# Kernel optimization log

Measured on AMD Instinct MI355X. Metric: run time of the kernel, lower is better.

Reference implementation:

```python
import jax, jax.numpy as jnp
import numpy as np

N_HEAD = 16

def setup_inputs() -> dict:
    key = jax.random.key(0)
    kx, kq, kk, kv, kp = jax.random.split(key, 5)
    B, T, C = 4, 2048, 1024
    scale = 1.0 / np.sqrt(C)
    x = jax.random.normal(kx, (B, T, C), dtype=jnp.float32)
    Wq = jax.random.normal(kq, (C, C), dtype=jnp.float32) * scale
    Wk = jax.random.normal(kk, (C, C), dtype=jnp.float32) * scale
    Wv = jax.random.normal(kv, (C, C), dtype=jnp.float32) * scale
    Wp = jax.random.normal(kp, (C, C), dtype=jnp.float32) * scale
    return {"x": x, "Wq": Wq, "Wk": Wk, "Wv": Wv, "Wp": Wp}

def reference(x, Wq, Wk, Wv, Wp):
    B, T, C = x.shape
    H = N_HEAD
    D = C // H
    # projections (nn.Linear, no bias): x @ W^T
    q = (x @ Wq.T).reshape(B, T, H, D).transpose(0, 2, 1, 3)  # [B,H,T,D]
    k = (x @ Wk.T).reshape(B, T, H, D).transpose(0, 2, 1, 3)
    v = (x @ Wv.T).reshape(B, T, H, D).transpose(0, 2, 1, 3)
    att = jnp.einsum('bhqd,bhkd->bhqk', q, k) / jnp.sqrt(jnp.float32(D))
    causal = jnp.tril(jnp.ones((T, T), dtype=bool))
    att = jnp.where(causal, att, -jnp.inf)
    att = jax.nn.softmax(att, axis=-1)
    # dropout p=0.0 -> identity
    y = jnp.einsum('bhqk,bhkd->bhqd', att, v)  # [B,H,T,D]
    y = y.transpose(0, 2, 1, 3).reshape(B, T, C)
    return y @ Wp.T
```

## Files before the change

kernel.cpp:

```cpp
#include <hip/hip_runtime.h>

typedef __bf16 bfrag __attribute__((ext_vector_type(8)));
typedef __bf16 bh4 __attribute__((ext_vector_type(4)));
typedef float f4 __attribute__((ext_vector_type(4)));

#define AS1C(p) (const __attribute__((address_space(1))) void*)(p)
#define AS3(p)  (__attribute__((address_space(3))) void*)(p)

#define QSCALE 0.18033688011112042f

__device__ __forceinline__ void g2l16(const __bf16* g, __bf16* l) {
  __builtin_amdgcn_global_load_lds(AS1C(g), AS3(l), 16, 0, 0);
}

__global__ __launch_bounds__(256) void cvt5(
    const float* __restrict__ s0, const float* __restrict__ s1,
    const float* __restrict__ s2, const float* __restrict__ s3,
    const float* __restrict__ s4,
    __bf16* __restrict__ d0, __bf16* __restrict__ d1, __bf16* __restrict__ d2,
    __bf16* __restrict__ d3, __bf16* __restrict__ d4, long n0, long n1) {
  const float* s; __bf16* d; long n;
  switch (blockIdx.y) {
    case 0: s = s0; d = d0; n = n0; break;
    case 1: s = s1; d = d1; n = n1; break;
    case 2: s = s2; d = d2; n = n1; break;
    case 3: s = s3; d = d3; n = n1; break;
    default: s = s4; d = d4; n = n1; break;
  }
  long i = ((long)blockIdx.x * 256 + threadIdx.x) * 8;
  if (i >= n) return;
  float4 a = *(const float4*)(s + i);
  float4 b = *(const float4*)(s + i + 4);
  bfrag o;
  o[0] = (__bf16)a.x; o[1] = (__bf16)a.y; o[2] = (__bf16)a.z; o[3] = (__bf16)a.w;
  o[4] = (__bf16)b.x; o[5] = (__bf16)b.y; o[6] = (__bf16)b.z; o[7] = (__bf16)b.w;
  *(bfrag*)(d + i) = o;
}

__global__ __launch_bounds__(256) void gemm_qkv(
    const __bf16* __restrict__ A, const __bf16* __restrict__ B,
    __bf16* __restrict__ qb, __bf16* __restrict__ kb, __bf16* __restrict__ vt,
    int M, int K) {
  __shared__ __bf16 sbuf[16640];
  __bf16* As0 = sbuf;
  __bf16* As1 = sbuf + 4096;
  __bf16* Bs0 = sbuf + 8192;
  __bf16* Bs1 = sbuf + 12288;
  const int tid = threadIdx.x;
  const int wave = tid >> 6, lane = tid & 63;
  const int lm = lane & 15, quad = lane >> 4;
  const int bm = blockIdx.x * 128, bn = blockIdx.y * 128;
  const int wr = (wave >> 1) * 64, wc = (wave & 1) * 64;
  f4 acc[4][4] = {};
  for (int k0 = 0; k0 < K; k0 += 64) {
#pragma unroll
    for (int ii = 0; ii < 2; ++ii) {
      int s = ii * 4 + wave;
      int e = s * 512 + lane * 8;
      int r = e >> 5, c = e & 31;
      const __bf16* ar = A + (long)(bm + r) * K + k0 + c;
      const __bf16* br = B + (long)(bn + r) * K + k0 + c;
      g2l16(ar, As0 + e);
      g2l16(ar + 32, As1 + e);
      g2l16(br, Bs0 + e);
      g2l16(br + 32, Bs1 + e);
    }
    __syncthreads();
#pragma unroll
    for (int st = 0; st < 2; ++st) {
      const __bf16* As = st ? As1 : As0;
      const __bf16* Bs = st ? Bs1 : Bs0;
      bfrag af[4], bg[4];
#pragma unroll
      for (int mi = 0; mi < 4; ++mi)
        af[mi] = *(const bfrag*)(As + (wr + mi * 16 + lm) * 32 + quad * 8);
#pragma unroll
      for (int ni = 0; ni < 4; ++ni)
        bg[ni] = *(const bfrag*)(Bs + (wc + ni * 16 + lm) * 32 + quad * 8);
#pragma unroll
      for (int mi = 0; mi < 4; ++mi)
#pragma unroll
        for (int ni = 0; ni < 4; ++ni)
          acc[mi][ni] = __builtin_amdgcn_mfma_f32_16x16x32_bf16(af[mi], bg[ni], acc[mi][ni], 0, 0, 0);
    }
    __syncthreads();
  }
  if (bn < 2048) {
    __bf16* dst = (bn < 1024) ? qb : kb;
    const float scl = (bn < 1024) ? QSCALE : 1.0f;
    const int nb = bn & 1023;
#pragma unroll
    for (int mi = 0; mi < 4; ++mi)
#pragma unroll
      for (int ni = 0; ni < 4; ++ni)
#pragma unroll
        for (int r = 0; r < 4; ++r) {
          long row = bm + wr + mi * 16 + quad * 4 + r;
          long col = nb + wc + ni * 16 + lm;
          dst[row * 1024 + col] = (__bf16)(acc[mi][ni][r] * scl);
        }
  } else {
#pragma unroll
    for (int mi = 0; mi < 4; ++mi)
#pragma unroll
      for (int ni = 0; ni < 4; ++ni)
#pragma unroll
        for (int r = 0; r < 4; ++r) {
          int d = wc + ni * 16 + lm;
          int tp = (wr ? 64 : 0) + (quad * 4 + r) * 4 + mi;
          sbuf[d * 130 + tp] = (__bf16)acc[mi][ni][r];
        }
    __syncthreads();
    const int bloc = bm >> 11;
    const int tloc = bm & 2047;
#pragma unroll
    for (int p = 0; p < 8; ++p) {
      int d = (tid >> 4) + p * 16;
      int c = (tid & 15) * 8;
      long dglob = (bn - 2048) + d;
      *(bfrag*)(vt + ((long)bloc * 1024 + dglob) * 2048 + tloc + c) =
          *(const bfrag*)(sbuf + d * 130 + c);
    }
  }
}

template <bool OUT_F32>
__global__ __launch_bounds__(256) void gemm_bt_bf16(
    const __bf16* __restrict__ A, const __bf16* __restrict__ B,
    void* __restrict__ Cp, int M, int N, int K) {
  __shared__ __bf16 sbuf[16384];
  __bf16* As0 = sbuf;
  __bf16* As1 = sbuf + 4096;
  __bf16* Bs0 = sbuf + 8192;
  __bf16* Bs1 = sbuf + 12288;
  const int tid = threadIdx.x;
  const int wave = tid >> 6, lane = tid & 63;
  const int lm = lane & 15, quad = lane >> 4;
  const int bm = blockIdx.x * 128, bn = blockIdx.y * 128;
  const int wr = (wave >> 1) * 64, wc = (wave & 1) * 64;
  f4 acc[4][4] = {};
  for (int k0 = 0; k0 < K; k0 += 64) {
#pragma unroll
    for (int ii = 0; ii < 2; ++ii) {
      int s = ii * 4 + wave;
      int e = s * 512 + lane * 8;
      int r = e >> 5, c = e & 31;
      const __bf16* ar = A + (long)(bm + r) * K + k0 + c;
      const __bf16* br = B + (long)(bn + r) * K + k0 + c;
      g2l16(ar, As0 + e);
      g2l16(ar + 32, As1 + e);
      g2l16(br, Bs0 + e);
      g2l16(br + 32, Bs1 + e);
    }
    __syncthreads();
#pragma unroll
    for (int st = 0; st < 2; ++st) {
      const __bf16* As = st ? As1 : As0;
      const __bf16* Bs = st ? Bs1 : Bs0;
      bfrag af[4], bg[4];
#pragma unroll
      for (int mi = 0; mi < 4; ++mi)
        af[mi] = *(const bfrag*)(As + (wr + mi * 16 + lm) * 32 + quad * 8);
#pragma unroll
      for (int ni = 0; ni < 4; ++ni)
        bg[ni] = *(const bfrag*)(Bs + (wc + ni * 16 + lm) * 32 + quad * 8);
#pragma unroll
      for (int mi = 0; mi < 4; ++mi)
#pragma unroll
        for (int ni = 0; ni < 4; ++ni)
          acc[mi][ni] = __builtin_amdgcn_mfma_f32_16x16x32_bf16(af[mi], bg[ni], acc[mi][ni], 0, 0, 0);
    }
    __syncthreads();
  }
#pragma unroll
  for (int mi = 0; mi < 4; ++mi)
#pragma unroll
    for (int ni = 0; ni < 4; ++ni)
#pragma unroll
      for (int r = 0; r < 4; ++r) {
        long row = bm + wr + mi * 16 + quad * 4 + r;
        long col = bn + wc + ni * 16 + lm;
        if (OUT_F32) ((float*)Cp)[row * N + col] = acc[mi][ni][r];
        else ((__bf16*)Cp)[row * N + col] = (__bf16)acc[mi][ni][r];
      }
}

template <bool A_F32, bool OUT_F32>
__global__ __launch_bounds__(256) void gemm_bt_cv(
    const void* __restrict__ Ap, const float* __restrict__ Bp,
    void* __restrict__ Cp, int M, int N, int K, float scl) {
  __shared__ __bf16 As[128 * 32];
  __shared__ __bf16 Bs[128 * 32];
  const int tid = threadIdx.x;
  const int lane = tid & 63, wave = tid >> 6;
  const int lm = lane & 15, quad = lane >> 4;
  const int bm = blockIdx.x * 128, bn = blockIdx.y * 128;
  const int wr = (wave >> 1) * 64, wc = (wave & 1) * 64;
  const int e0 = tid * 16, sr = e0 >> 5, sc = e0 & 31;
  f4 acc[4][4] = {};
  for (int k0 = 0; k0 < K; k0 += 32) {
    if (A_F32) {
      const float4* ga = (const float4*)((const float*)Ap + (long)(bm + sr) * K + k0 + sc);
#pragma unroll
      for (int j = 0; j < 4; ++j) {
        float4 v = ga[j];
        As[sr * 32 + sc + j * 4 + 0] = (__bf16)v.x;
        As[sr * 32 + sc + j * 4 + 1] = (__bf16)v.y;
        As[sr * 32 + sc + j * 4 + 2] = (__bf16)v.z;
        As[sr * 32 + sc + j * 4 + 3] = (__bf16)v.w;
      }
    } else {
      const __bf16* Ab = (const __bf16*)Ap + (long)(bm + sr) * K + k0 + sc;
      *(bfrag*)(As + sr * 32 + sc) = *(const bfrag*)Ab;
      *(bfrag*)(As + sr * 32 + sc + 8) = *(const bfrag*)(Ab + 8);
    }
    {
      const float4* gb = (const float4*)(Bp + (long)(bn + sr) * K + k0 + sc);
#pragma unroll
      for (int j = 0; j < 4; ++j) {
        float4 v = gb[j];
        Bs[sr * 32 + sc + j * 4 + 0] = (__bf16)v.x;
        Bs[sr * 32 + sc + j * 4 + 1] = (__bf16)v.y;
        Bs[sr * 32 + sc + j * 4 + 2] = (__bf16)v.z;
        Bs[sr * 32 + sc + j * 4 + 3] = (__bf16)v.w;
      }
    }
    __syncthreads();
    bfrag af[4], bg[4];
#pragma unroll
    for (int mi = 0; mi < 4; ++mi)
      af[mi] = *(const bfrag*)(As + (wr + mi * 16 + lm) * 32 + quad * 8);
#pragma unroll
    for (int ni = 0; ni < 4; ++ni)
      bg[ni] = *(const bfrag*)(Bs + (wc + ni * 16 + lm) * 32 + quad * 8);
#pragma unroll
    for (int mi = 0; mi < 4; ++mi)
#pragma unroll
      for (int ni = 0; ni < 4; ++ni)
        acc[mi][ni] = __builtin_amdgcn_mfma_f32_16x16x32_bf16(af[mi], bg[ni], acc[mi][ni], 0, 0, 0);
    __syncthreads();
  }
#pragma unroll
  for (int mi = 0; mi < 4; ++mi)
#pragma unroll
    for (int ni = 0; ni < 4; ++ni)
#pragma unroll
      for (int r = 0; r < 4; ++r) {
        long row = bm + wr + mi * 16 + quad * 4 + r;
        long col = bn + wc + ni * 16 + lm;
        if (OUT_F32) ((float*)Cp)[row * N + col] = acc[mi][ni][r] * scl;
        else ((__bf16*)Cp)[row * N + col] = (__bf16)(acc[mi][ni][r] * scl);
      }
}

#define KP 72

template <bool DIAG>
__device__ __forceinline__ void attn_tile(
    const bfrag* qf, int row0, int kBase,
    const bfrag* kf, const bfrag* vf, __bf16* Psw,
    int lm, int quad, f4* yacc, f4& Lacc, bfrag ones) {
  f4 sac[4];
#pragma unroll
  for (int sub = 0; sub < 4; ++sub) {
    f4 z = {};
#pragma unroll
    for (int f = 0; f < 2; ++f)
      z = __builtin_amdgcn_mfma_f32_16x16x32_bf16(qf[f], kf[sub * 2 + f], z, 0, 0, 0);
    sac[sub] = z;
  }
#pragma unroll
  for (int r = 0; r < 4; ++r) {
    bh4 pk;
#pragma unroll
    for (int sub = 0; sub < 4; ++sub) {
      float pv = __builtin_amdgcn_exp2f(sac[sub][r]);
      if (DIAG) {
        bool masked = (kBase + sub * 16 + lm > row0 + quad * 4 + r);
        pv = masked ? 0.f : pv;
      }
      pk[sub] = (__bf16)pv;
    }
    *(bh4*)(Psw + (quad * 4 + r) * KP + lm * 4) = pk;
  }
  __asm__ volatile("s_waitcnt lgkmcnt(0)" ::: "memory");
#pragma unroll
  for (int f = 0; f < 2; ++f) {
    bfrag pf = *(const bfrag*)(Psw + lm * KP + f * 32 + quad * 8);
    Lacc = __builtin_amdgcn_mfma_f32_16x16x32_bf16(pf, ones, Lacc, 0, 0, 0);
#pragma unroll
    for (int ds = 0; ds < 4; ++ds)
      yacc[ds] = __builtin_amdgcn_mfma_f32_16x16x32_bf16(pf, vf[ds * 2 + f], yacc[ds], 0, 0, 0);
  }
}

template <bool DIAG_A>
__device__ __forceinline__ void attn_tile2(
    const bfrag* qfA, const bfrag* qfB, int rowA0, int kBase,
    const bfrag* kf, const bfrag* vf, __bf16* PswA, __bf16* PswB,
    int lm, int quad, f4* yA, f4* yB, f4& LA, f4& LB, bfrag ones) {
  f4 sA[4], sB[4];
#pragma unroll
  for (int sub = 0; sub < 4; ++sub) {
    f4 za = {}, zb = {};
#pragma unroll
    for (int f = 0; f < 2; ++f) {
      za = __builtin_amdgcn_mfma_f32_16x16x32_bf16(qfA[f], kf[sub * 2 + f], za, 0, 0, 0);
      zb = __builtin_amdgcn_mfma_f32_16x16x32_bf16(qfB[f], kf[sub * 2 + f], zb, 0, 0, 0);
    }
    sA[sub] = za; sB[sub] = zb;
  }
#pragma unroll
  for (int r = 0; r < 4; ++r) {
    bh4 pa, pb;
#pragma unroll
    for (int sub = 0; sub < 4; ++sub) {
      float va = __builtin_amdgcn_exp2f(sA[sub][r]);
      if (DIAG_A) {
        bool masked = (kBase + sub * 16 + lm > rowA0 + quad * 4 + r);
        va = masked ? 0.f : va;
      }
      pa[sub] = (__bf16)va;
      pb[sub] = (__bf16)__builtin_amdgcn_exp2f(sB[sub][r]);
    }
    *(bh4*)(PswA + (quad * 4 + r) * KP + lm * 4) = pa;
    *(bh4*)(PswB + (quad * 4 + r) * KP + lm * 4) = pb;
  }
  __asm__ volatile("s_waitcnt lgkmcnt(0)" ::: "memory");
#pragma unroll
  for (int f = 0; f < 2; ++f) {
    bfrag pfa = *(const bfrag*)(PswA + lm * KP + f * 32 + quad * 8);
    bfrag pfb = *(const bfrag*)(PswB + lm * KP + f * 32 + quad * 8);
    LA = __builtin_amdgcn_mfma_f32_16x16x32_bf16(pfa, ones, LA, 0, 0, 0);
    LB = __builtin_amdgcn_mfma_f32_16x16x32_bf16(pfb, ones, LB, 0, 0, 0);
#pragma unroll
    for (int ds = 0; ds < 4; ++ds) {
      yA[ds] = __builtin_amdgcn_mfma_f32_16x16x32_bf16(pfa, vf[ds * 2 + f], yA[ds], 0, 0, 0);
      yB[ds] = __builtin_amdgcn_mfma_f32_16x16x32_bf16(pfb, vf[ds * 2 + f], yB[ds], 0, 0, 0);
    }
  }
}

template <bool VT>
__global__ __launch_bounds__(256) void attn_fwd7(
    const __bf16* Qg, const __bf16* __restrict__ Kg,
    const __bf16* __restrict__ Vsrc, __bf16* Yg) {
  const int TT = 2048, CC = 1024;
  __shared__ __bf16 Ks[64 * KP];
  __shared__ __bf16 Vs[64 * KP];
  __shared__ __bf16 Ps[8 * 16 * KP];
  const int tid = threadIdx.x;
  const int wave = tid >> 6, lane = tid & 63;
  const int lm = lane & 15, quad = lane >> 4;
  const int i = blockIdx.x;
  const int qtA = i, qtB = 31 - i;
  const int b = blockIdx.y >> 4, h = blockIdx.y & 15;
  const long rbase = (long)b * TT;
  const int hoff = h * 64;
  const int rowA0 = qtA * 64 + wave * 16, rowB0 = qtB * 64 + wave * 16;
  bfrag qfA[2], qfB[2];
#pragma unroll
  for (int f = 0; f < 2; ++f) {
    qfA[f] = *(const bfrag*)(Qg + (rbase + rowA0 + lm) * CC + hoff + f * 32 + quad * 8);
    qfB[f] = *(const bfrag*)(Qg + (rbase + rowB0 + lm) * CC + hoff + f * 32 + quad * 8);
  }
  bfrag ones;
#pragma unroll
  for (int j = 0; j < 8; ++j) ones[j] = (__bf16)1.0f;
  f4 yA[4] = {}, yB[4] = {};
  f4 LA = {}, LB = {};
  __bf16* PswA = Ps + wave * 16 * KP;
  __bf16* PswB = Ps + (wave + 4) * 16 * KP;
  for (int kt = 0; kt <= qtB; ++kt) {
    const int kBase = kt * 64;
    __syncthreads();
#pragma unroll
    for (int s = 0; s < 2; ++s) {
      int idx = tid + s * 256;
      int r = idx >> 3, c = (idx & 7) * 8;
      *(bfrag*)(Ks + r * KP + c) =
          *(const bfrag*)(Kg + (rbase + kBase + r) * CC + hoff + c);
    }
    if (VT) {
#pragma unroll
      for (int s = 0; s < 2; ++s) {
        int idx = tid + s * 256;
        int d = idx >> 3, kc = (idx & 7) * 8;
        *(bfrag*)(Vs + d * KP + kc) =
            *(const bfrag*)(Vsrc + ((long)b * 1024 + hoff + d) * 2048 + kBase + kc);
      }
    } else {
#pragma unroll
      for (int s = 0; s < 2; ++s) {
        int idx = tid + s * 256;
        int r = idx >> 3, c = (idx & 7) * 8;
        int kp = (r & 15) * 4 + (r >> 4);
        bfrag vv = *(const bfrag*)(Vsrc + (rbase + kBase + r) * CC + hoff + c);
#pragma unroll
        for (int j = 0; j < 8; ++j) Vs[(c + j) * KP + kp] = vv[j];
      }
    }
    __syncthreads();
    bfrag kf[8], vf[8];
#pragma unroll
    for (int sub = 0; sub < 4; ++sub)
#pragma unroll
      for (int f = 0; f < 2; ++f) {
        kf[sub * 2 + f] = *(const bfrag*)(Ks + (sub * 16 + lm) * KP + f * 32 + quad * 8);
        vf[sub * 2 + f] = *(const bfrag*)(Vs + (sub * 16 + lm) * KP + f * 32 + quad * 8);
      }
    if (kt < qtA)
      attn_tile2<false>(qfA, qfB, rowA0, kBase, kf, vf, PswA, PswB, lm, quad, yA, yB, LA, LB, ones);
    else if (kt == qtA)
      attn_tile2<true>(qfA, qfB, rowA0, kBase, kf, vf, PswA, PswB, lm, quad, yA, yB, LA, LB, ones);
    else if (kt < qtB)
      attn_tile<false>(qfB, rowB0, kBase, kf, vf, PswB, lm, quad, yB, LB, ones);
    else
      attn_tile<true>(qfB, rowB0, kBase, kf, vf, PswB, lm, quad, yB, LB, ones);
  }
#pragma unroll
  for (int ds = 0; ds < 4; ++ds)
#pragma unroll
    for (int r = 0; r < 4; ++r) {
      long rowa = rbase + rowA0 + quad * 4 + r;
      long rowb = rbase + rowB0 + quad * 4 + r;
      Yg[rowa * CC + hoff + ds * 16 + lm] = (__bf16)(yA[ds][r] / LA[r]);
      Yg[rowb * CC + hoff + ds * 16 + lm] = (__bf16)(yB[ds][r] / LB[r]);
    }
}

extern "C" void kernel_launch(void* const* d_in, const int* in_sizes, int n_in,
                              void* d_out, int out_size, void* d_ws, size_t ws_size,
                              hipStream_t stream) {
  (void)in_sizes; (void)n_in; (void)out_size;
  const float* x  = (const float*)d_in[0];
  const float* Wq = (const float*)d_in[1];
  const float* Wk = (const float*)d_in[2];
  const float* Wv = (const float*)d_in[3];
  const float* Wp = (const float*)d_in[4];
  float* out = (float*)d_out;
  const long R = 8192;
  const long BUF = R * 1024;
  const long WN = 1024L * 1024;
  __bf16* qb = (__bf16*)d_ws;
  __bf16* kb = (__bf16*)d_out;
  __bf16* vslot = kb + BUF;
  dim3 blk(256, 1, 1);
  const size_t need = (size_t)(2 * BUF + 4 * WN) * 2;
  if (ws_size >= need) {
    __bf16* xb = qb + BUF;
    __bf16* wqkv = xb + BUF;
    __bf16* wpb = wqkv + 3 * WN;
    cvt5<<<dim3((unsigned)(BUF / (256 * 8)), 5, 1), blk, 0, stream>>>(
        x, Wq, Wk, Wv, Wp, xb, wqkv, wqkv + WN, wqkv + 2 * WN, wpb, BUF, WN);
    gemm_qkv<<<dim3(64, 24, 1), blk, 0, stream>>>(xb, wqkv, qb, kb, vslot, 8192, 1024);
    attn_fwd7<true><<<dim3(16, 64, 1), blk, 0, stream>>>(qb, kb, vslot, qb);
    gemm_bt_bf16<true><<<dim3(64, 8, 1), blk, 0, stream>>>(qb, wpb, out, 8192, 1024, 1024);
  } else {
    gemm_bt_cv<true, false><<<dim3(64, 8, 1), blk, 0, stream>>>(x, Wq, qb, 8192, 1024, 1024, QSCALE);
    gemm_bt_cv<true, false><<<dim3(64, 8, 1), blk, 0, stream>>>(x, Wk, kb, 8192, 1024, 1024, 1.0f);
    gemm_bt_cv<true, false><<<dim3(64, 8, 1), blk, 0, stream>>>(x, Wv, vslot, 8192, 1024, 1024, 1.0f);
    attn_fwd7<false><<<dim3(16, 64, 1), blk, 0, stream>>>(qb, kb, vslot, qb);
    gemm_bt_cv<false, true><<<dim3(64, 8, 1), blk, 0, stream>>>(qb, Wp, out, 8192, 1024, 1024, 1.0f);
  }
}
```

Baseline: 264.1 us.

## Process 128-row query tile pairs per block with register-prefetched K/V tiles

The attention kernel now gives each block two 128-row query tiles (four 16-row fragments per wave) instead of two 64-row tiles. Each loaded K/V tile is reused across twice as many query rows, and the grid shrinks to 512 blocks ordered by batch-head first. It also prefetches the next K/V tile into registers while the current one is being computed, and adds a launch bound asking for two blocks per CU. In exchange it holds more accumulators and Q fragments in registers and uses a larger P scratch buffer in shared memory, which may reduce occupancy or cause register spills. It also leaves fewer blocks to balance across CUs.

```diff
diff --git a/kernel.cpp b/kernel.cpp
--- a/kernel.cpp
+++ b/kernel.cpp
@@ -255,178 +255,163 @@
 
 #define KP 72
 
-template <bool DIAG>
-__device__ __forceinline__ void attn_tile(
-    const bfrag* qf, int row0, int kBase,
-    const bfrag* kf, const bfrag* vf, __bf16* Psw,
-    int lm, int quad, f4* yacc, f4& Lacc, bfrag ones) {
-  f4 sac[4];
-#pragma unroll
-  for (int sub = 0; sub < 4; ++sub) {
-    f4 z = {};
-#pragma unroll
-    for (int f = 0; f < 2; ++f)
-      z = __builtin_amdgcn_mfma_f32_16x16x32_bf16(qf[f], kf[sub * 2 + f], z, 0, 0, 0);
-    sac[sub] = z;
-  }
-#pragma unroll
-  for (int r = 0; r < 4; ++r) {
-    bh4 pk;
-#pragma unroll
-    for (int sub = 0; sub < 4; ++sub) {
-      float pv = __builtin_amdgcn_exp2f(sac[sub][r]);
-      if (DIAG) {
-        bool masked = (kBase + sub * 16 + lm > row0 + quad * 4 + r);
-        pv = masked ? 0.f : pv;
-      }
-      pk[sub] = (__bf16)pv;
-    }
-    *(bh4*)(Psw + (quad * 4 + r) * KP + lm * 4) = pk;
-  }
-  __asm__ volatile("s_waitcnt lgkmcnt(0)" ::: "memory");
-#pragma unroll
-  for (int f = 0; f < 2; ++f) {
-    bfrag pf = *(const bfrag*)(Psw + lm * KP + f * 32 + quad * 8);
-    Lacc = __builtin_amdgcn_mfma_f32_16x16x32_bf16(pf, ones, Lacc, 0, 0, 0);
-#pragma unroll
-    for (int ds = 0; ds < 4; ++ds)
-      yacc[ds] = __builtin_amdgcn_mfma_f32_16x16x32_bf16(pf, vf[ds * 2 + f], yacc[ds], 0, 0, 0);
-  }
-}
-
-template <bool DIAG_A>
-__device__ __forceinline__ void attn_tile2(
-    const bfrag* qfA, const bfrag* qfB, int rowA0, int kBase,
-    const bfrag* kf, const bfrag* vf, __bf16* PswA, __bf16* PswB,
-    int lm, int quad, f4* yA, f4* yB, f4& LA, f4& LB, bfrag ones) {
-  f4 sA[4], sB[4];
-#pragma unroll
-  for (int sub = 0; sub < 4; ++sub) {
-    f4 za = {}, zb = {};
-#pragma unroll
-    for (int f = 0; f < 2; ++f) {
-      za = __builtin_amdgcn_mfma_f32_16x16x32_bf16(qfA[f], kf[sub * 2 + f], za, 0, 0, 0);
-      zb = __builtin_amdgcn_mfma_f32_16x16x32_bf16(qfB[f], kf[sub * 2 + f], zb, 0, 0, 0);
-    }
-    sA[sub] = za; sB[sub] = zb;
-  }
-#pragma unroll
-  for (int r = 0; r < 4; ++r) {
-    bh4 pa, pb;
-#pragma unroll
-    for (int sub = 0; sub < 4; ++sub) {
-      float va = __builtin_amdgcn_exp2f(sA[sub][r]);
-      if (DIAG_A) {
-        bool masked = (kBase + sub * 16 + lm > rowA0 + quad * 4 + r);
-        va = masked ? 0.f : va;
-      }
-      pa[sub] = (__bf16)va;
-      pb[sub] = (__bf16)__builtin_amdgcn_exp2f(sB[sub][r]);
-    }
-    *(bh4*)(PswA + (quad * 4 + r) * KP + lm * 4) = pa;
-    *(bh4*)(PswB + (quad * 4 + r) * KP + lm * 4) = pb;
-  }
-  __asm__ volatile("s_waitcnt lgkmcnt(0)" ::: "memory");
-#pragma unroll
-  for (int f = 0; f < 2; ++f) {
-    bfrag pfa = *(const bfrag*)(PswA + lm * KP + f * 32 + quad * 8);
-    bfrag pfb = *(const bfrag*)(PswB + lm * KP + f * 32 + quad * 8);
-    LA = __builtin_amdgcn_mfma_f32_16x16x32_bf16(pfa, ones, LA, 0, 0, 0);
-    LB = __builtin_amdgcn_mfma_f32_16x16x32_bf16(pfb, ones, LB, 0, 0, 0);
-#pragma unroll
-    for (int ds = 0; ds < 4; ++ds) {
-      yA[ds] = __builtin_amdgcn_mfma_f32_16x16x32_bf16(pfa, vf[ds * 2 + f], yA[ds], 0, 0, 0);
-      yB[ds] = __builtin_amdgcn_mfma_f32_16x16x32_bf16(pfb, vf[ds * 2 + f], yB[ds], 0, 0, 0);
-    }
-  }
-}
-
 template <bool VT>
-__global__ __launch_bounds__(256) void attn_fwd7(
+__global__ __launch_bounds__(256, 2) void attn_fwd8(
     const __bf16* Qg, const __bf16* __restrict__ Kg,
     const __bf16* __restrict__ Vsrc, __bf16* Yg) {
   const int TT = 2048, CC = 1024;
   __shared__ __bf16 Ks[64 * KP];
   __shared__ __bf16 Vs[64 * KP];
-  __shared__ __bf16 Ps[8 * 16 * KP];
+  __shared__ __bf16 Ps[16 * 16 * KP];
   const int tid = threadIdx.x;
   const int wave = tid >> 6, lane = tid & 63;
   const int lm = lane & 15, quad = lane >> 4;
-  const int i = blockIdx.x;
-  const int qtA = i, qtB = 31 - i;
-  const int b = blockIdx.y >> 4, h = blockIdx.y & 15;
+  const int bh = blockIdx.x, i = blockIdx.y;
+  const int b = bh >> 4, h = bh & 15;
+  const int qtA = i, qtB = 15 - i;
   const long rbase = (long)b * TT;
   const int hoff = h * 64;
-  const int rowA0 = qtA * 64 + wave * 16, rowB0 = qtB * 64 + wave * 16;
-  bfrag qfA[2], qfB[2];
-#pragma unroll
-  for (int f = 0; f < 2; ++f) {
-    qfA[f] = *(const bfrag*)(Qg + (rbase + rowA0 + lm) * CC + hoff + f * 32 + quad * 8);
-    qfB[f] = *(const bfrag*)(Qg + (rbase + rowB0 + lm) * CC + hoff + f * 32 + quad * 8);
-  }
+  int row0[4];
+  row0[0] = qtA * 128 + wave * 16;
+  row0[1] = qtA * 128 + 64 + wave * 16;
+  row0[2] = qtB * 128 + wave * 16;
+  row0[3] = qtB * 128 + 64 + wave * 16;
+  __bf16* Pw[4];
+#pragma unroll
+  for (int fr = 0; fr < 4; ++fr) Pw[fr] = Ps + (wave * 4 + fr) * 16 * KP;
+  bfrag qf[4][2];
+#pragma unroll
+  for (int fr = 0; fr < 4; ++fr)
+#pragma unroll
+    for (int f = 0; f < 2; ++f)
+      qf[fr][f] = *(const bfrag*)(Qg + (rbase + row0[fr] + lm) * CC + hoff + f * 32 + quad * 8);
   bfrag ones;
 #pragma unroll
   for (int j = 0; j < 8; ++j) ones[j] = (__bf16)1.0f;
-  f4 yA[4] = {}, yB[4] = {};
-  f4 LA = {}, LB = {};
-  __bf16* PswA = Ps + wave * 16 * KP;
-  __bf16* PswB = Ps + (wave + 4) * 16 * KP;
-  for (int kt = 0; kt <= qtB; ++kt) {
+  f4 y[4][4] = {};
+  f4 L[4] = {};
+
+  const int ktLast = 2 * qtB + 1;
+  bfrag kin[2], vin[2];
+#pragma unroll
+  for (int s = 0; s < 2; ++s) {
+    int idx = tid + s * 256;
+    int r = idx >> 3, c = (idx & 7) * 8;
+    kin[s] = *(const bfrag*)(Kg + (rbase + r) * CC + hoff + c);
+    if (VT)
+      vin[s] = *(const bfrag*)(Vsrc + ((long)b * 1024 + hoff + r) * 2048 + c);
+    else
+      vin[s] = *(const bfrag*)(Vsrc + (rbase + r) * CC + hoff + c);
+  }
+
+  for (int kt = 0; kt <= ktLast; ++kt) {
     const int kBase = kt * 64;
     __syncthreads();
 #pragma unroll
     for (int s = 0; s < 2; ++s) {
       int idx = tid + s * 256;
       int r = idx >> 3, c = (idx & 7) * 8;
-      *(bfrag*)(Ks + r * KP + c) =
-          *(const bfrag*)(Kg + (rbase + kBase + r) * CC + hoff + c);
-    }
-    if (VT) {
-#pragma unroll
-      for (int s = 0; s < 2; ++s) {
-        int idx = tid + s * 256;
-        int d = idx >> 3, kc = (idx & 7) * 8;
-        *(bfrag*)(Vs + d * KP + kc) =
-            *(const bfrag*)(Vsrc + ((long)b * 1024 + hoff + d) * 2048 + kBase + kc);
-      }
-    } else {
+      *(bfrag*)(Ks + r * KP + c) = kin[s];
+      if (VT) {
+        *(bfrag*)(Vs + r * KP + c) = vin[s];
+      } else {
+        int kp = (r & 15) * 4 + (r >> 4);
+#pragma unroll
+        for (int j = 0; j < 8; ++j) Vs[(c + j) * KP + kp] = vin[s][j];
+      }
+    }
+    const bool more = (kt < ktLast);
+    bfrag kin2[2], vin2[2];
+    if (more) {
+      const int nB = kBase + 64;
 #pragma unroll
       for (int s = 0; s < 2; ++s) {
         int idx = tid + s * 256;
         int r = idx >> 3, c = (idx & 7) * 8;
-        int kp = (r & 15) * 4 + (r >> 4);
-        bfrag vv = *(const bfrag*)(Vsrc + (rbase + kBase + r) * CC + hoff + c);
-#pragma unroll
-        for (int j = 0; j < 8; ++j) Vs[(c + j) * KP + kp] = vv[j];
-      }
-    }
-    __syncthreads();
-    bfrag kf[8], vf[8];
+        kin2[s] = *(const bfrag*)(Kg + (rbase + nB + r) * CC + hoff + c);
+        if (VT)
+          vin2[s] = *(const bfrag*)(Vsrc + ((long)b * 1024 + hoff + r) * 2048 + nB + c);
+        else
+          vin2[s] = *(const bfrag*)(Vsrc + (rbase + nB + r) * CC + hoff + c);
+      }
+    }
+    __syncthreads();
+    bfrag kf[8];
 #pragma unroll
     for (int sub = 0; sub < 4; ++sub)
 #pragma unroll
-      for (int f = 0; f < 2; ++f) {
+      for (int f = 0; f < 2; ++f)
         kf[sub * 2 + f] = *(const bfrag*)(Ks + (sub * 16 + lm) * KP + f * 32 + quad * 8);
+#pragma unroll
+    for (int fr = 0; fr < 4; ++fr) {
+      if (kBase <= row0[fr] + 15) {
+        f4 sac[4];
+#pragma unroll
+        for (int sub = 0; sub < 4; ++sub) {
+          f4 z = {};
+#pragma unroll
+          for (int f = 0; f < 2; ++f)
+            z = __builtin_amdgcn_mfma_f32_16x16x32_bf16(qf[fr][f], kf[sub * 2 + f], z, 0, 0, 0);
+          sac[sub] = z;
+        }
+        if (kBase + 63 > row0[fr]) {
+#pragma unroll
+          for (int r = 0; r < 4; ++r) {
+            bh4 pk;
+#pragma unroll
+            for (int sub = 0; sub < 4; ++sub) {
+              float pv = __builtin_amdgcn_exp2f(sac[sub][r]);
+              bool masked = (kBase + sub * 16 + lm > row0[fr] + quad * 4 + r);
+              pk[sub] = (__bf16)(masked ? 0.f : pv);
+            }
+            *(bh4*)(Pw[fr] + (quad * 4 + r) * KP + lm * 4) = pk;
+          }
+        } else {
+#pragma unroll
+          for (int r = 0; r < 4; ++r) {
+            bh4 pk;
+#pragma unroll
+            for (int sub = 0; sub < 4; ++sub)
+              pk[sub] = (__bf16)__builtin_amdgcn_exp2f(sac[sub][r]);
+            *(bh4*)(Pw[fr] + (quad * 4 + r) * KP + lm * 4) = pk;
+          }
+        }
+      }
+    }
+    __asm__ volatile("s_waitcnt lgkmcnt(0)" ::: "memory");
+    bfrag vf[8];
+#pragma unroll
+    for (int sub = 0; sub < 4; ++sub)
+#pragma unroll
+      for (int f = 0; f < 2; ++f)
         vf[sub * 2 + f] = *(const bfrag*)(Vs + (sub * 16 + lm) * KP + f * 32 + quad * 8);
-      }
-    if (kt < qtA)
-      attn_tile2<false>(qfA, qfB, rowA0, kBase, kf, vf, PswA, PswB, lm, quad, yA, yB, LA, LB, ones);
-    else if (kt == qtA)
-      attn_tile2<true>(qfA, qfB, rowA0, kBase, kf, vf, PswA, PswB, lm, quad, yA, yB, LA, LB, ones);
-    else if (kt < qtB)
-      attn_tile<false>(qfB, rowB0, kBase, kf, vf, PswB, lm, quad, yB, LB, ones);
-    else
-      attn_tile<true>(qfB, rowB0, kBase, kf, vf, PswB, lm, quad, yB, LB, ones);
-  }
-#pragma unroll
-  for (int ds = 0; ds < 4; ++ds)
-#pragma unroll
-    for (int r = 0; r < 4; ++r) {
-      long rowa = rbase + rowA0 + quad * 4 + r;
-      long rowb = rbase + rowB0 + quad * 4 + r;
-      Yg[rowa * CC + hoff + ds * 16 + lm] = (__bf16)(yA[ds][r] / LA[r]);
-      Yg[rowb * CC + hoff + ds * 16 + lm] = (__bf16)(yB[ds][r] / LB[r]);
-    }
+#pragma unroll
+    for (int fr = 0; fr < 4; ++fr) {
+      if (kBase <= row0[fr] + 15) {
+#pragma unroll
+        for (int f = 0; f < 2; ++f) {
+          bfrag pf = *(const bfrag*)(Pw[fr] + lm * KP + f * 32 + quad * 8);
+          L[fr] = __builtin_amdgcn_mfma_f32_16x16x32_bf16(pf, ones, L[fr], 0, 0, 0);
+#pragma unroll
+          for (int ds = 0; ds < 4; ++ds)
+            y[fr][ds] = __builtin_amdgcn_mfma_f32_16x16x32_bf16(pf, vf[ds * 2 + f], y[fr][ds], 0, 0, 0);
+        }
+      }
+    }
+    if (more) {
+      kin[0] = kin2[0]; kin[1] = kin2[1];
+      vin[0] = vin2[0]; vin[1] = vin2[1];
+    }
+  }
+#pragma unroll
+  for (int fr = 0; fr < 4; ++fr)
+#pragma unroll
+    for (int ds = 0; ds < 4; ++ds)
+#pragma unroll
+      for (int r = 0; r < 4; ++r) {
+        long row = rbase + row0[fr] + quad * 4 + r;
+        Yg[row * CC + hoff + ds * 16 + lm] = (__bf16)(y[fr][ds][r] / L[fr][r]);
+      }
 }
 
 extern "C" void kernel_launch(void* const* d_in, const int* in_sizes, int n_in,
@@ -454,13 +439,13 @@
     cvt5<<<dim3((unsigned)(BUF / (256 * 8)), 5, 1), blk, 0, stream>>>(
         x, Wq, Wk, Wv, Wp, xb, wqkv, wqkv + WN, wqkv + 2 * WN, wpb, BUF, WN);
     gemm_qkv<<<dim3(64, 24, 1), blk, 0, stream>>>(xb, wqkv, qb, kb, vslot, 8192, 1024);
-    attn_fwd7<true><<<dim3(16, 64, 1), blk, 0, stream>>>(qb, kb, vslot, qb);
+    attn_fwd8<true><<<dim3(64, 8, 1), blk, 0, stream>>>(qb, kb, vslot, qb);
     gemm_bt_bf16<true><<<dim3(64, 8, 1), blk, 0, stream>>>(qb, wpb, out, 8192, 1024, 1024);
   } else {
     gemm_bt_cv<true, false><<<dim3(64, 8, 1), blk, 0, stream>>>(x, Wq, qb, 8192, 1024, 1024, QSCALE);
     gemm_bt_cv<true, false><<<dim3(64, 8, 1), blk, 0, stream>>>(x, Wk, kb, 8192, 1024, 1024, 1.0f);
     gemm_bt_cv<true, false><<<dim3(64, 8, 1), blk, 0, stream>>>(x, Wv, vslot, 8192, 1024, 1024, 1.0f);
-    attn_fwd7<false><<<dim3(16, 64, 1), blk, 0, stream>>>(qb, kb, vslot, qb);
+    attn_fwd8<false><<<dim3(64, 8, 1), blk, 0, stream>>>(qb, kb, vslot, qb);
     gemm_bt_cv<false, true><<<dim3(64, 8, 1), blk, 0, stream>>>(qb, Wp, out, 8192, 1024, 1024, 1.0f);
   }
 }
```

Measured after the change: 229.2 us. 1.15x faster.
